# Optimization experiments

Measured on AMD Instinct MI355X. Metric: run time of the kernel, lower is better.

Reference implementation:

```python
import jax, jax.numpy as jnp
import numpy as np

B, T, C, HS = 1024, 128, 384, 64


def setup_inputs() -> dict:
    key = jax.random.key(0)
    k1, k2, k3, k4 = jax.random.split(key, 4)
    std = 1.0 / np.sqrt(C)  # ~ nn.Linear default init scale
    return {
        "x": jax.random.normal(k1, (B, T, C), dtype=jnp.float32),
        "Wq": jax.random.normal(k2, (C, HS), dtype=jnp.float32) * std,
        "Wk": jax.random.normal(k3, (C, HS), dtype=jnp.float32) * std,
        "Wv": jax.random.normal(k4, (C, HS), dtype=jnp.float32) * std,
    }


def reference(x, Wq, Wk, Wv):
    # x: [B, T, C]; Wq/Wk/Wv: [C, HS]
    q = jnp.einsum("btc,ch->bth", x, Wq)
    k = jnp.einsum("btc,ch->bth", x, Wk)
    v = jnp.einsum("btc,ch->bth", x, Wv)
    scale = 1.0 / jnp.sqrt(jnp.asarray(k.shape[-1], dtype=x.dtype))
    wei = jnp.einsum("bth,bsh->bts", q, k) * scale  # [B, T, T]
    t = x.shape[1]
    causal = jnp.tril(jnp.ones((t, t), dtype=bool))
    wei = jnp.where(causal, wei, jnp.asarray(-jnp.inf, dtype=wei.dtype))
    wei = jax.nn.softmax(wei, axis=-1)
    # dropout omitted (eval mode / deterministic reference)
    out = jnp.einsum("bts,bsh->bth", wei, v)  # [B, T, HS]
    return out
```

## Files before the change

kernel.cpp:

```cpp
#include <hip/hip_runtime.h>


typedef __attribute__((ext_vector_type(8)))  short  short8;
typedef __attribute__((ext_vector_type(16))) float  floatx16;
typedef __attribute__((ext_vector_type(4)))  float  float4v;

#define T_DIM   128
#define C_DIM   384
#define HS      64
#define NCHUNK  12
#define SLAB    1536

#define QK_PITCH 68
#define V_PITCH  132
#define P_PITCH  132
#define Q_OFF  0
#define K_OFF  17408
#define XV_OFF 34816
#define LDS_BYTES 51712
#define P_OFF  0

#define MFMA(a,b,c) __builtin_amdgcn_mfma_f32_32x32x16_bf16((a),(b),(c),0,0,0)

__device__ inline unsigned short f2bf(float f){
    unsigned u = __builtin_bit_cast(unsigned, f);
    u += 0x7FFFu + ((u >> 16) & 1u);
    return (unsigned short)(u >> 16);
}

__device__ inline short8 ld_b64x2(const char* p){
    union { unsigned long long u[2]; short8 s; } r;
    r.u[0] = *(const unsigned long long*)(p);
    r.u[1] = *(const unsigned long long*)(p + 8);
    return r.s;
}

__global__ void prep_wt(const float* __restrict__ Wq, const float* __restrict__ Wk,
                        const float* __restrict__ Wv, unsigned short* __restrict__ wt){
    int idx = blockIdx.x * 256 + threadIdx.x;
    if (idx >= 48 * SLAB) return;
    int slab = idx / SLAB;
    int rem  = idx - slab * SLAB;
    int n = rem >> 3, j = rem & 7;
    int half = slab & 1, ks = (slab >> 1) & 1, c = slab >> 2;
    int kg = c*32 + ks*16 + half*8 + j;
    const float* W = (n < 64) ? Wq : (n < 128) ? Wk : Wv;
    wt[idx] = f2bf(W[kg * HS + (n & 63)]);
}

__launch_bounds__(256, 3)
__global__ void attn_kernel(const float* __restrict__ x,
                            const unsigned short* __restrict__ wtg,
                            float* __restrict__ out){
    __shared__ __align__(16) char smem[LDS_BYTES];
    const int tid  = threadIdx.x;
    const int lane = tid & 63;
    const int wave = tid >> 6;
    const int l31  = lane & 31;
    const int half = lane >> 5;
    const int koff = half * 8;
    const int b    = blockIdx.x;
    const char* xb = (const char*)(x + (size_t)b * (T_DIM * C_DIM));

    const short8* wf = (const short8*)wtg;
    floatx16 acc[6] = {};

    const char* gsrc[4];
    #pragma unroll
    for (int i = 0; i < 4; ++i){
        int o  = wave*1024 + i*4096 + lane*16;
        int t  = o >> 7;
        int pp = ((o >> 4) & 7) ^ (t & 7);
        gsrc[i] = xb + t*1536 + pp*16;
    }
    const int xrow_base = XV_OFF + (32*wave + l31) * 128;
    const int rs = (32*wave + l31) & 7;

    for (int c = 0; c < NCHUNK; ++c){
        __syncthreads();
        #pragma unroll
        for (int i = 0; i < 4; ++i){
            __builtin_amdgcn_global_load_lds(
                (const __attribute__((address_space(1))) void*)(gsrc[i] + c*128),
                (__attribute__((address_space(3))) void*)(smem + XV_OFF + wave*1024 + i*4096),
                16, 0, 0);
        }
        __syncthreads();

        short8 afrag[2];
        #pragma unroll
        for (int ks = 0; ks < 2; ++ks){
            int q0 = ks*4 + half*2;
            float4v lo = *(const float4v*)(smem + xrow_base + ((q0  ) ^ rs)*16);
            float4v hi = *(const float4v*)(smem + xrow_base + ((q0+1) ^ rs)*16);
            short8 a;
            a[0]=(short)f2bf(lo[0]); a[1]=(short)f2bf(lo[1]);
            a[2]=(short)f2bf(lo[2]); a[3]=(short)f2bf(lo[3]);
            a[4]=(short)f2bf(hi[0]); a[5]=(short)f2bf(hi[1]);
            a[6]=(short)f2bf(hi[2]); a[7]=(short)f2bf(hi[3]);
            afrag[ks] = a;
        }
        #pragma unroll
        for (int ks = 0; ks < 2; ++ks){
            const short8* slab = wf + ((c*2 + ks)*2 + half) * 192;
            #pragma unroll
            for (int nbl = 0; nbl < 6; ++nbl){
                short8 bfrag = slab[32*nbl + l31];
                acc[nbl] = MFMA(afrag[ks], bfrag, acc[nbl]);
            }
        }
    }
    __syncthreads();

    const float QSCALE = 0.125f * 1.44269504088896f;
    #pragma unroll
    for (int nb = 0; nb < 6; ++nb){
        floatx16 A = acc[nb];
        if (nb < 4){
            int base  = (nb < 2) ? Q_OFF : K_OFF;
            int col   = 32 * (nb & 1) + l31;
            float sc  = (nb < 2) ? QSCALE : 1.0f;
            char* bp  = smem + base + col * 2;
            #pragma unroll
            for (int r = 0; r < 16; ++r){
                int t = 32*wave + (r&3) + 8*(r>>2) + 4*half;
                *(unsigned short*)(bp + t * (QK_PITCH*2)) = f2bf(A[r] * sc);
            }
        } else {
            int h = 32*(nb-4) + l31;
            char* bp = smem + XV_OFF + h * (V_PITCH*2);
            #pragma unroll
            for (int g = 0; g < 4; ++g){
                int t0 = 32*wave + 8*g + 4*half;
                union { unsigned short s[4]; unsigned long long u; } pk;
                pk.s[0]=f2bf(A[4*g+0]); pk.s[1]=f2bf(A[4*g+1]);
                pk.s[2]=f2bf(A[4*g+2]); pk.s[3]=f2bf(A[4*g+3]);
                *(unsigned long long*)(bp + t0*2) = pk.u;
            }
        }
    }
    __syncthreads();

    floatx16 accS[4] = {};
    #pragma unroll
    for (int ks = 0; ks < 4; ++ks){
        short8 aq = ld_b64x2(smem + Q_OFF + (32*wave + l31)*(QK_PITCH*2) + (ks*16 + koff)*2);
        #pragma unroll
        for (int st = 0; st < 4; ++st)
            if (st <= wave){
                short8 bk = ld_b64x2(smem + K_OFF + (32*st + l31)*(QK_PITCH*2) + (ks*16 + koff)*2);
                accS[st] = MFMA(aq, bk, accS[st]);
            }
    }
    #pragma unroll
    for (int st = 0; st < 4; ++st)
        if (st <= wave){
            #pragma unroll
            for (int r = 0; r < 16; ++r){
                int trow = (r&3) + 8*(r>>2) + 4*half;
                float e = exp2f(accS[st][r]);
                if (st == wave && l31 > trow) e = 0.0f;
                accS[st][r] = e;
            }
        }

    float linv[16];
    #pragma unroll
    for (int r = 0; r < 16; ++r){
        float l = accS[0][r] + accS[1][r] + accS[2][r] + accS[3][r];
        #pragma unroll
        for (int m = 1; m <= 16; m <<= 1)
            l += __shfl_xor(l, m);
        linv[r] = 1.0f / l;
    }
    __syncthreads();

    #pragma unroll
    for (int st = 0; st < 4; ++st)
        if (st <= wave){
            char* bp = smem + P_OFF + (32*st + l31) * 2;
            #pragma unroll
            for (int r = 0; r < 16; ++r){
                int t = 32*wave + (r&3) + 8*(r>>2) + 4*half;
                *(unsigned short*)(bp + t * (P_PITCH*2)) = f2bf(accS[st][r]);
            }
        }
    __syncthreads();

    floatx16 accO0 = {}, accO1 = {};
    const int nks = 2 * (wave + 1);
    #pragma unroll
    for (int ks = 0; ks < 8; ++ks)
        if (ks < nks){
            short8 ap  = ld_b64x2(smem + P_OFF + (32*wave + l31)*(P_PITCH*2) + (ks*16 + koff)*2);
            short8 bv0 = ld_b64x2(smem + XV_OFF + l31        *(V_PITCH*2) + (ks*16 + koff)*2);
            short8 bv1 = ld_b64x2(smem + XV_OFF + (l31 + 32) *(V_PITCH*2) + (ks*16 + koff)*2);
            accO0 = MFMA(ap, bv0, accO0);
            accO1 = MFMA(ap, bv1, accO1);
        }

    float* ob = out + (size_t)b * (T_DIM * HS);
    #pragma unroll
    for (int r = 0; r < 16; ++r){
        int t = 32*wave + (r&3) + 8*(r>>2) + 4*half;
        ob[t*HS + l31]      = accO0[r] * linv[r];
        ob[t*HS + l31 + 32] = accO1[r] * linv[r];
    }
}

extern "C" void kernel_launch(void* const* d_in, const int* in_sizes, int n_in,
                              void* d_out, int out_size, void* d_ws, size_t ws_size,
                              hipStream_t stream){
    const float* x  = (const float*)d_in[0];
    const float* Wq = (const float*)d_in[1];
    const float* Wk = (const float*)d_in[2];
    const float* Wv = (const float*)d_in[3];
    unsigned short* wt = (unsigned short*)d_ws;

    prep_wt<<<288, 256, 0, stream>>>(Wq, Wk, Wv, wt);
    attn_kernel<<<1024, 256, 0, stream>>>(x, wt, (float*)d_out);
}
```

Before: 317.3 us.

## Split fused attention into QKV projection and attention kernels via global workspace

Splits the single fused kernel into two. The first computes the Q/K/V projections and writes them as bf16 to a global workspace in an MFMA-fragment-friendly layout. The second reads Q/K/V fragments directly from global memory, keeps only the P tile in shared memory, and drops two block barriers. This unfusion is meant to let each kernel use its own LDS budget and schedule, which could improve occupancy for the attention part, at the cost of an extra kernel launch and a global write and read of about 48 KB per batch.

```diff
diff --git a/kernel.cpp b/kernel.cpp
--- a/kernel.cpp
+++ b/kernel.cpp
@@ -17,8 +17,11 @@
 #define Q_OFF  0
 #define K_OFF  17408
 #define XV_OFF 34816
-#define LDS_BYTES 51712
-#define P_OFF  0
+#define LDS_A  51712
+#define LDS_B  33792
+
+#define QKV_OFF_SHORTS 73728
+#define QKV_PER_B      24576
 
 #define MFMA(a,b,c) __builtin_amdgcn_mfma_f32_32x32x16_bf16((a),(b),(c),0,0,0)
 
@@ -49,16 +52,15 @@
 }
 
 __launch_bounds__(256, 3)
-__global__ void attn_kernel(const float* __restrict__ x,
-                            const unsigned short* __restrict__ wtg,
-                            float* __restrict__ out){
-    __shared__ __align__(16) char smem[LDS_BYTES];
+__global__ void qkv_kernel(const float* __restrict__ x,
+                           const unsigned short* __restrict__ wtg,
+                           unsigned short* __restrict__ qkvg){
+    __shared__ __align__(16) char smem[LDS_A];
     const int tid  = threadIdx.x;
     const int lane = tid & 63;
     const int wave = tid >> 6;
     const int l31  = lane & 31;
     const int half = lane >> 5;
-    const int koff = half * 8;
     const int b    = blockIdx.x;
     const char* xb = (const char*)(x + (size_t)b * (T_DIM * C_DIM));
 
@@ -141,14 +143,62 @@
     }
     __syncthreads();
 
+    unsigned short* qkv = qkvg + (size_t)b * QKV_PER_B;
+    #pragma unroll
+    for (int i = 0; i < 4; ++i){
+        int e = tid + 256*i;
+        int t = e & 127, kh = e >> 7;
+        const char* src = smem + Q_OFF + t*(QK_PITCH*2) + kh*16;
+        union { unsigned long long u[2]; float4v v; } r;
+        r.u[0] = *(const unsigned long long*)src;
+        r.u[1] = *(const unsigned long long*)(src + 8);
+        *(float4v*)(qkv + e*8) = r.v;
+    }
+    #pragma unroll
+    for (int i = 0; i < 4; ++i){
+        int e = tid + 256*i;
+        int t = e & 127, kh = e >> 7;
+        const char* src = smem + K_OFF + t*(QK_PITCH*2) + kh*16;
+        union { unsigned long long u[2]; float4v v; } r;
+        r.u[0] = *(const unsigned long long*)src;
+        r.u[1] = *(const unsigned long long*)(src + 8);
+        *(float4v*)(qkv + 8192 + e*8) = r.v;
+    }
+    #pragma unroll
+    for (int i = 0; i < 4; ++i){
+        int e = tid + 256*i;
+        int h = e & 63, kh = e >> 6;
+        const char* src = smem + XV_OFF + h*(V_PITCH*2) + kh*16;
+        union { unsigned long long u[2]; float4v v; } r;
+        r.u[0] = *(const unsigned long long*)src;
+        r.u[1] = *(const unsigned long long*)(src + 8);
+        *(float4v*)(qkv + 16384 + e*8) = r.v;
+    }
+}
+
+__launch_bounds__(256, 3)
+__global__ void attn2_kernel(const unsigned short* __restrict__ qkvg,
+                             float* __restrict__ out){
+    __shared__ __align__(16) char smem[LDS_B];
+    const int tid  = threadIdx.x;
+    const int lane = tid & 63;
+    const int wave = tid >> 6;
+    const int l31  = lane & 31;
+    const int half = lane >> 5;
+    const int koff = half * 8;
+    const int b    = blockIdx.x;
+    const short8* qf = (const short8*)(qkvg + (size_t)b * QKV_PER_B);
+    const short8* kf = qf + 1024;
+    const short8* vf = qf + 2048;
+
     floatx16 accS[4] = {};
     #pragma unroll
     for (int ks = 0; ks < 4; ++ks){
-        short8 aq = ld_b64x2(smem + Q_OFF + (32*wave + l31)*(QK_PITCH*2) + (ks*16 + koff)*2);
+        short8 aq = qf[(ks*2+half)*128 + 32*wave + l31];
         #pragma unroll
         for (int st = 0; st < 4; ++st)
             if (st <= wave){
-                short8 bk = ld_b64x2(smem + K_OFF + (32*st + l31)*(QK_PITCH*2) + (ks*16 + koff)*2);
+                short8 bk = kf[(ks*2+half)*128 + 32*st + l31];
                 accS[st] = MFMA(aq, bk, accS[st]);
             }
     }
@@ -173,28 +223,26 @@
             l += __shfl_xor(l, m);
         linv[r] = 1.0f / l;
     }
-    __syncthreads();
 
     #pragma unroll
     for (int st = 0; st < 4; ++st)
         if (st <= wave){
-            char* bp = smem + P_OFF + (32*st + l31) * 2;
+            char* bp = smem + (32*st + l31) * 2;
             #pragma unroll
             for (int r = 0; r < 16; ++r){
                 int t = 32*wave + (r&3) + 8*(r>>2) + 4*half;
                 *(unsigned short*)(bp + t * (P_PITCH*2)) = f2bf(accS[st][r]);
             }
         }
-    __syncthreads();
 
     floatx16 accO0 = {}, accO1 = {};
     const int nks = 2 * (wave + 1);
     #pragma unroll
     for (int ks = 0; ks < 8; ++ks)
         if (ks < nks){
-            short8 ap  = ld_b64x2(smem + P_OFF + (32*wave + l31)*(P_PITCH*2) + (ks*16 + koff)*2);
-            short8 bv0 = ld_b64x2(smem + XV_OFF + l31        *(V_PITCH*2) + (ks*16 + koff)*2);
-            short8 bv1 = ld_b64x2(smem + XV_OFF + (l31 + 32) *(V_PITCH*2) + (ks*16 + koff)*2);
+            short8 ap  = ld_b64x2(smem + (32*wave + l31)*(P_PITCH*2) + (ks*16 + koff)*2);
+            short8 bv0 = vf[(ks*2+half)*64 + l31];
+            short8 bv1 = vf[(ks*2+half)*64 + l31 + 32];
             accO0 = MFMA(ap, bv0, accO0);
             accO1 = MFMA(ap, bv1, accO1);
         }
@@ -215,8 +263,10 @@
     const float* Wq = (const float*)d_in[1];
     const float* Wk = (const float*)d_in[2];
     const float* Wv = (const float*)d_in[3];
-    unsigned short* wt = (unsigned short*)d_ws;
+    unsigned short* wt   = (unsigned short*)d_ws;
+    unsigned short* qkvg = wt + QKV_OFF_SHORTS;
 
     prep_wt<<<288, 256, 0, stream>>>(Wq, Wk, Wv, wt);
-    attn_kernel<<<1024, 256, 0, stream>>>(x, wt, (float*)d_out);
-}
+    qkv_kernel<<<1024, 256, 0, stream>>>(x, wt, qkvg);
+    attn2_kernel<<<1024, 256, 0, stream>>>(qkvg, (float*)d_out);
+}
```

Result: slower. 331.1 us (+4.3%).
